# Optimization experiments

Hardware: AMD Instinct MI355X
Metric: run time of the kernel (lower is better)

## Reference

```python
import jax, jax.numpy as jnp
import numpy as np

B, T = 64, 200
NUM_C2 = 2000
NUM_D = 1000
V = 128

# NOTE: Dropout layers are identity in eval mode; this reference implements eval-mode forward.

def setup_inputs() -> dict:
    key = jax.random.key(0)
    ks = jax.random.split(key, 19)
    s = 0.05
    def nrm(k, shape):
        return jax.random.normal(k, shape, jnp.float32) * s
    return {
        "c_seq": jax.random.randint(ks[0], (B, T), 0, NUM_C2),
        "d_seq": jax.random.randint(ks[1], (B, T), 0, NUM_D),
        "r_seq": (jax.random.uniform(ks[2], (B, T)) < 0.5).astype(jnp.float32),
        "D_emb": nrm(ks[3], (NUM_D, 1)),
        "v_d": nrm(ks[4], (V,)),
        "v_r": nrm(ks[5], (V,)),
        "v_c": nrm(ks[6], (V,)),
        "W_ih": nrm(ks[7], (3 * V, 2 * V)),
        "W_hh": nrm(ks[8], (3 * V, V)),
        "b_ih": nrm(ks[9], (3 * V,)),
        "b_hh": nrm(ks[10], (3 * V,)),
        "W1a": nrm(ks[11], (V, V)),
        "b1a": nrm(ks[12], (V,)),
        "W1b": nrm(ks[13], (1, V)),
        "b1b": nrm(ks[14], (1,)),
        "W2a": nrm(ks[15], (V, 3 * V)),
        "b2a": nrm(ks[16], (V,)),
        "W2b": nrm(ks[17], (1, V)),
        "b2b": nrm(ks[18], (1,)),
    }


def reference(c_seq, d_seq, r_seq, D_emb, v_d, v_r, v_c,
              W_ih, W_hh, b_ih, b_hh, W1a, b1a, W1b, b1b,
              W2a, b2a, W2b, b2b):
    gamma_seq = D_emb[d_seq]                 # [B,T,1]
    v_d_seq = gamma_seq * v_d                # [B,T,V]
    v_r_seq = r_seq[..., None] * v_r         # [B,T,V]
    x = jnp.concatenate([v_d_seq, v_r_seq], axis=-1)  # [B,T,2V]

    # --- GRU (PyTorch gate ordering r,z,n), h0 = 0 ---
    def gru_step(h, x_t):
        gi = x_t @ W_ih.T + b_ih
        gh = h @ W_hh.T + b_hh
        i_r, i_z, i_n = jnp.split(gi, 3, axis=-1)
        h_r, h_z, h_n = jnp.split(gh, 3, axis=-1)
        r = jax.nn.sigmoid(i_r + h_r)
        z = jax.nn.sigmoid(i_z + h_z)
        n = jnp.tanh(i_n + r * h_n)
        h_new = (1.0 - z) * n + z * h
        return h_new, h_new

    h0 = jnp.zeros((c_seq.shape[0], v_d.shape[0]), x.dtype)
    _, h_seq = jax.lax.scan(gru_step, h0, jnp.swapaxes(x, 0, 1))
    h_seq = jnp.swapaxes(h_seq, 0, 1)        # [B,T,V]

    # linear_1 (dropout = identity in eval)
    alpha_seq = (jax.nn.relu(h_seq @ W1a.T + b1a) @ W1b.T + b1b)[..., 0]  # [B,T]

    # --- sequential memory update over time ---
    def mem_step(C, inputs):
        c_t, vd_t, vr_t = inputs             # [B], [B,V], [B,V]
        beta = jnp.take_along_axis(C, c_t[:, None], axis=1)   # [B,1]
        vc = beta * v_c                       # [B,V]
        hh = jax.nn.relu(jnp.concatenate([vc, vd_t, vr_t], axis=-1) @ W2a.T + b2a)
        new_c = hh @ W2b.T + b2b              # [B,1]
        oh = jax.nn.one_hot(c_t, C.shape[1], dtype=C.dtype)   # [B,K]
        C_new = C * (1.0 - oh) + new_c * oh
        return C_new, C_new

    C0 = jnp.zeros((c_seq.shape[0], NUM_C2), x.dtype)
    _, C_seq = jax.lax.scan(
        mem_step, C0,
        (jnp.swapaxes(c_seq, 0, 1), jnp.swapaxes(v_d_seq, 0, 1), jnp.swapaxes(v_r_seq, 0, 1)))
    C_seq = jnp.swapaxes(C_seq, 0, 1)[..., None]   # [B,T,K,1]
    return alpha_seq, h_seq, C_seq
```

## Files before the change

kernel.cpp:

```cpp
#include <hip/hip_runtime.h>
#include <hip/hip_bf16.h>
#include <cstdint>

#define BB 64
#define TT 200
#define KN 2000
#define VV 128
#define NGRU 16

typedef __attribute__((ext_vector_type(8))) short bf16x8;
typedef __attribute__((ext_vector_type(4))) float f32x4;
typedef _Float16 half8 __attribute__((ext_vector_type(8)));


__device__ __forceinline__ float sigm(float x) {
    return __builtin_amdgcn_rcpf(1.f + __expf(-x));
}
__device__ __forceinline__ float tanh_f(float x) {
    float e = __expf(2.f * x);
    return 1.f - 2.f * __builtin_amdgcn_rcpf(e + 1.f);
}

__device__ __forceinline__ void soft_barrier() {
    asm volatile("s_waitcnt lgkmcnt(0)" ::: "memory");
    __builtin_amdgcn_s_barrier();
    __builtin_amdgcn_sched_barrier(0);
}

__global__ void pre_kernel(const float* __restrict__ v_d, const float* __restrict__ v_r,
                           const float* __restrict__ v_c, const float* __restrict__ W_ih,
                           const float* __restrict__ W2a, float* __restrict__ ws)
{
    int g = blockIdx.x * 256 + threadIdx.x;
    float* pd = ws;
    float* pr = ws + 384;
    float* uc = ws + 768;
    float* ud = ws + 896;
    float* ur = ws + 1024;
    if (g < 384) {
        float a = 0.f, b = 0.f;
        for (int k = 0; k < VV; ++k) {
            a = fmaf(W_ih[g * 256 + k], v_d[k], a);
            b = fmaf(W_ih[g * 256 + VV + k], v_r[k], b);
        }
        pd[g] = a; pr[g] = b;
    }
    if (g < VV) {
        float a = 0.f, b = 0.f, c = 0.f;
        for (int k = 0; k < VV; ++k) {
            a = fmaf(W2a[g * 384 + k], v_c[k], a);
            b = fmaf(W2a[g * 384 + VV + k], v_d[k], b);
            c = fmaf(W2a[g * 384 + 2 * VV + k], v_r[k], c);
        }
        uc[g] = a; ud[g] = b; ur[g] = c;
    }
}

__device__ __forceinline__ half8 load_cvt8h(const float* p) {
    float4 a = *(const float4*)p;
    float4 c = *(const float4*)(p + 4);
    half8 r;
    r[0] = (_Float16)a.x; r[1] = (_Float16)a.y; r[2] = (_Float16)a.z; r[3] = (_Float16)a.w;
    r[4] = (_Float16)c.x; r[5] = (_Float16)c.y; r[6] = (_Float16)c.z; r[7] = (_Float16)c.w;
    return r;
}

__global__ __launch_bounds__(512, 1) void fused_kernel(
    const int* __restrict__ c_seq, const int* __restrict__ d_seq,
    const float* __restrict__ r_seq, const float* __restrict__ D_emb,
    const float* __restrict__ Whh, const float* __restrict__ bih,
    const float* __restrict__ bhh, const float* __restrict__ W2b,
    const float* __restrict__ b2a, const float* __restrict__ b2b,
    const float* __restrict__ ws, float* __restrict__ C_out,
    float* __restrict__ h_out)
{
    __shared__ __align__(16) _Float16 H_half[16 * 136];
    __shared__ __align__(8) float gam4[TT * 4], r4[TT * 4];
    __shared__ __align__(16) float C[KN];
    __shared__ float gam_row[TT], r_row[TT], n_row[TT];
    __shared__ int c_row[TT + 1];

    int tid = threadIdx.x;

    if (blockIdx.x < NGRU) {
        int b0 = blockIdx.x * 4;
        const float* pd = ws;
        const float* pr = ws + 384;

        for (int i = tid; i < TT * 4; i += 512) {
            int t = i >> 2, rr = i & 3;
            gam4[i] = D_emb[d_seq[(b0 + rr) * TT + t]];
            r4[i] = r_seq[(b0 + rr) * TT + t];
        }
        for (int i = tid; i < 16 * 136; i += 512) H_half[i] = (_Float16)0.f;

        int wid = tid >> 6, l = tid & 63;
        int cl = l & 15, gq = l >> 4;
        int nn = wid * 16 + cl;

        const float* wr = Whh + (size_t)nn * VV + gq * 8;
        const float* wz = Whh + (size_t)(nn + 128) * VV + gq * 8;
        const float* wn = Whh + (size_t)(nn + 256) * VV + gq * 8;
        half8 br0 = load_cvt8h(wr),      br1 = load_cvt8h(wr + 32),
              br2 = load_cvt8h(wr + 64), br3 = load_cvt8h(wr + 96);
        half8 bz0 = load_cvt8h(wz),      bz1 = load_cvt8h(wz + 32),
              bz2 = load_cvt8h(wz + 64), bz3 = load_cvt8h(wz + 96);
        half8 bn0 = load_cvt8h(wn),      bn1 = load_cvt8h(wn + 32),
              bn2 = load_cvt8h(wn + 64), bn3 = load_cvt8h(wn + 96);

        float gr_pd = pd[nn],        gr_pr = pr[nn],        gr_b = bih[nn] + bhh[nn];
        float gz_pd = pd[nn + 128],  gz_pr = pr[nn + 128],  gz_b = bih[nn + 128] + bhh[nn + 128];
        float gn_pd = pd[nn + 256],  gn_pr = pr[nn + 256],  gn_b = bih[nn + 256];
        float gn_bh = bhh[nn + 256];

        float h0 = 0.f;
        __syncthreads();

        for (int t = 0; t < TT; ++t) {
            asm volatile("" : "+v"(br0), "+v"(br1), "+v"(br2), "+v"(br3),
                              "+v"(bz0), "+v"(bz1), "+v"(bz2), "+v"(bz3),
                              "+v"(bn0), "+v"(bn1), "+v"(bn2), "+v"(bn3));
            const int ab = cl * 136 + gq * 8;
            half8 a0 = *(const half8*)&H_half[ab];
            half8 a1 = *(const half8*)&H_half[ab + 32];
            half8 a2 = *(const half8*)&H_half[ab + 64];
            half8 a3 = *(const half8*)&H_half[ab + 96];
            float g1 = gam4[t * 4 + gq];
            float q1 = r4[t * 4 + gq];

            f32x4 z4 = {0.f, 0.f, 0.f, 0.f};
            f32x4 accr = z4, accrh = z4, accz = z4, acczh = z4, accn = z4, accnh = z4;
            accr[0] = fmaf(g1, gr_pd, fmaf(q1, gr_pr, gr_b));
            accz[0] = fmaf(g1, gz_pd, fmaf(q1, gz_pr, gz_b));
            accn[0] = gn_bh;
            float gin0 = fmaf(g1, gn_pd, fmaf(q1, gn_pr, gn_b));

            accr  = __builtin_amdgcn_mfma_f32_16x16x32_f16(a0, br0, accr, 0, 0, 0);
            accrh = __builtin_amdgcn_mfma_f32_16x16x32_f16(a2, br2, accrh, 0, 0, 0);
            accz  = __builtin_amdgcn_mfma_f32_16x16x32_f16(a0, bz0, accz, 0, 0, 0);
            acczh = __builtin_amdgcn_mfma_f32_16x16x32_f16(a2, bz2, acczh, 0, 0, 0);
            accn  = __builtin_amdgcn_mfma_f32_16x16x32_f16(a0, bn0, accn, 0, 0, 0);
            accnh = __builtin_amdgcn_mfma_f32_16x16x32_f16(a2, bn2, accnh, 0, 0, 0);
            accr  = __builtin_amdgcn_mfma_f32_16x16x32_f16(a1, br1, accr, 0, 0, 0);
            accrh = __builtin_amdgcn_mfma_f32_16x16x32_f16(a3, br3, accrh, 0, 0, 0);
            accz  = __builtin_amdgcn_mfma_f32_16x16x32_f16(a1, bz1, accz, 0, 0, 0);
            acczh = __builtin_amdgcn_mfma_f32_16x16x32_f16(a3, bz3, acczh, 0, 0, 0);
            accn  = __builtin_amdgcn_mfma_f32_16x16x32_f16(a1, bn1, accn, 0, 0, 0);
            accnh = __builtin_amdgcn_mfma_f32_16x16x32_f16(a3, bn3, accnh, 0, 0, 0);

            {
                float rg0 = sigm(accr[0] + accrh[0]);
                float zg0 = sigm(accz[0] + acczh[0]);
                float ng0 = tanh_f(fmaf(rg0, accn[0] + accnh[0], gin0));
                h0 = fmaf(1.f - zg0, ng0, zg0 * h0);
                H_half[(gq * 4) * 136 + nn] = (_Float16)h0;
                h_out[((size_t)(b0 + gq) * TT + t) * VV + nn] = h0;
            }
            soft_barrier();
        }
    } else {
        int b = blockIdx.x - NGRU;
        const float* uc = ws + 768;
        const float* ud = ws + 896;
        const float* ur = ws + 1024;
        for (int i = tid; i < KN; i += 512) C[i] = 0.f;
        if (tid < TT) {
            gam_row[tid] = D_emb[d_seq[b * TT + tid]];
            r_row[tid] = r_seq[b * TT + tid];
            c_row[tid] = c_seq[b * TT + tid];
        }
        if (tid == 0) c_row[TT] = 0;
        __syncthreads();

        if (tid < 64) {
            int l = tid;
            float uc0 = uc[l], uc1 = uc[l + 64];
            float ud0 = ud[l], ud1 = ud[l + 64];
            float ur0 = ur[l], ur1 = ur[l + 64];
            float ba0 = b2a[l], ba1 = b2a[l + 64];
            float wb0 = W2b[l], wb1 = W2b[l + 64];
            float bb = b2b[0];
            float beta = 0.f;
            int ct = c_row[0];
            for (int t = 0; t < TT; ++t) {
                int ct1 = c_row[t + 1];
                float cpref = C[ct1];
                float g = gam_row[t], rr = r_row[t];
                float hh0 = fmaxf(fmaf(beta, uc0, fmaf(g, ud0, fmaf(rr, ur0, ba0))), 0.f);
                float hh1 = fmaxf(fmaf(beta, uc1, fmaf(g, ud1, fmaf(rr, ur1, ba1))), 0.f);
                float p = fmaf(hh0, wb0, hh1 * wb1);
                #pragma unroll
                for (int m = 32; m > 0; m >>= 1) p += __shfl_xor(p, m);
                float nc = p + bb;
                if (l == 0) { C[ct] = nc; n_row[t] = nc; }
                beta = (ct1 == ct) ? nc : cpref;
                ct = ct1;
            }
        }
        __syncthreads();

        int k0 = tid * 4;
        if (k0 < KN) {
            float4 cur = {0.f, 0.f, 0.f, 0.f};
            float* cop = C_out + (size_t)b * TT * KN + k0;
            for (int t = 0; t < TT; ++t) {
                int c = c_row[t];
                unsigned d = (unsigned)(c - k0);
                if (d < 4u) {
                    float v = n_row[t];
                    cur.x = (d == 0u) ? v : cur.x;
                    cur.y = (d == 1u) ? v : cur.y;
                    cur.z = (d == 2u) ? v : cur.z;
                    cur.w = (d == 3u) ? v : cur.w;
                }
                *(float4*)(cop + (size_t)t * KN) = cur;
            }
        }
    }
}

__device__ __forceinline__ short f2bf(float f) {
    uint32_t u = __float_as_uint(f);
    u = (u + 0x7FFFu + ((u >> 16) & 1u)) >> 16;
    return (short)u;
}
__device__ __forceinline__ bf16x8 load_cvt8(const float* p) {
    float4 a = *(const float4*)p;
    float4 c = *(const float4*)(p + 4);
    bf16x8 r;
    r[0] = f2bf(a.x); r[1] = f2bf(a.y); r[2] = f2bf(a.z); r[3] = f2bf(a.w);
    r[4] = f2bf(c.x); r[5] = f2bf(c.y); r[6] = f2bf(c.z); r[7] = f2bf(c.w);
    return r;
}

__global__ __launch_bounds__(512) void alpha_kernel(
    const float* __restrict__ h_seq, const float* __restrict__ W1a,
    const float* __restrict__ b1a, const float* __restrict__ W1b,
    const float* __restrict__ b1b, float* __restrict__ alpha)
{
    __shared__ __align__(16) short W1s[128 * 136];
    __shared__ float b1s[128], w1bs[128];
    int tid = threadIdx.x;
    for (int i = tid * 8; i < 128 * 128; i += 512 * 8) {
        int row = i >> 7, col = i & 127;
        *(bf16x8*)&W1s[row * 136 + col] = load_cvt8(W1a + i);
    }
    if (tid < 128) { b1s[tid] = b1a[tid]; w1bs[tid] = W1b[tid]; }
    __syncthreads();

    int wave = tid >> 6, lane = tid & 63;
    int tile = blockIdx.x * 8 + wave;
    int rowbase = tile * 16;
    int rl = lane & 15, g = lane >> 4;
    const float* hp = h_seq + (size_t)(rowbase + rl) * VV + g * 8;
    bf16x8 a0 = load_cvt8(hp);
    bf16x8 a1 = load_cvt8(hp + 32);
    bf16x8 a2 = load_cvt8(hp + 64);
    bf16x8 a3 = load_cvt8(hp + 96);
    float p0 = 0.f, p1 = 0.f, p2 = 0.f, p3 = 0.f;
    float bb = b1b[0];
    #pragma unroll
    for (int jt = 0; jt < 8; ++jt) {
        int j = jt * 16 + rl;
        const short* wp = &W1s[j * 136 + g * 8];
        f32x4 acc = {0.f, 0.f, 0.f, 0.f};
        acc = __builtin_amdgcn_mfma_f32_16x16x32_bf16(a0, *(const bf16x8*)wp, acc, 0, 0, 0);
        acc = __builtin_amdgcn_mfma_f32_16x16x32_bf16(a1, *(const bf16x8*)(wp + 32), acc, 0, 0, 0);
        acc = __builtin_amdgcn_mfma_f32_16x16x32_bf16(a2, *(const bf16x8*)(wp + 64), acc, 0, 0, 0);
        acc = __builtin_amdgcn_mfma_f32_16x16x32_bf16(a3, *(const bf16x8*)(wp + 96), acc, 0, 0, 0);
        float bj = b1s[j], wj = w1bs[j];
        p0 += fmaxf(acc[0] + bj, 0.f) * wj;
        p1 += fmaxf(acc[1] + bj, 0.f) * wj;
        p2 += fmaxf(acc[2] + bj, 0.f) * wj;
        p3 += fmaxf(acc[3] + bj, 0.f) * wj;
    }
    #pragma unroll
    for (int m = 1; m < 16; m <<= 1) {
        p0 += __shfl_xor(p0, m);
        p1 += __shfl_xor(p1, m);
        p2 += __shfl_xor(p2, m);
        p3 += __shfl_xor(p3, m);
    }
    if (rl == 0) {
        alpha[rowbase + g * 4 + 0] = p0 + bb;
        alpha[rowbase + g * 4 + 1] = p1 + bb;
        alpha[rowbase + g * 4 + 2] = p2 + bb;
        alpha[rowbase + g * 4 + 3] = p3 + bb;
    }
}

extern "C" void kernel_launch(void* const* d_in, const int* in_sizes, int n_in,
                              void* d_out, int out_size, void* d_ws, size_t ws_size,
                              hipStream_t stream)
{
    const int*   c_seq = (const int*)d_in[0];
    const int*   d_seq = (const int*)d_in[1];
    const float* r_seq = (const float*)d_in[2];
    const float* D_emb = (const float*)d_in[3];
    const float* v_d   = (const float*)d_in[4];
    const float* v_r   = (const float*)d_in[5];
    const float* v_c   = (const float*)d_in[6];
    const float* W_ih  = (const float*)d_in[7];
    const float* W_hh  = (const float*)d_in[8];
    const float* b_ih  = (const float*)d_in[9];
    const float* b_hh  = (const float*)d_in[10];
    const float* W1a   = (const float*)d_in[11];
    const float* b1a   = (const float*)d_in[12];
    const float* W1b   = (const float*)d_in[13];
    const float* b1b   = (const float*)d_in[14];
    const float* W2a   = (const float*)d_in[15];
    const float* b2a   = (const float*)d_in[16];
    const float* W2b   = (const float*)d_in[17];
    const float* b2b   = (const float*)d_in[18];

    float* out   = (float*)d_out;
    float* alpha = out;
    float* h_seq = out + 12800;
    float* C_out = out + 12800 + 1638400;
    float* ws    = (float*)d_ws;

    hipLaunchKernelGGL(pre_kernel, dim3(2), dim3(256), 0, stream,
                       v_d, v_r, v_c, W_ih, W2a, ws);
    hipLaunchKernelGGL(fused_kernel, dim3(NGRU + BB), dim3(512), 0, stream,
                       c_seq, d_seq, r_seq, D_emb, W_hh, b_ih, b_hh,
                       W2b, b2a, b2b, ws, C_out, h_seq);
    hipLaunchKernelGGL(alpha_kernel, dim3(100), dim3(512), 0, stream,
                       h_seq, W1a, b1a, W1b, b1b, alpha);
}
```

Measured before the change: 117.8 us.

## Halve GRU block size with two hidden-column tiles per wave

New measurement: 136.5 us. 15.9% more time.

```diff
diff --git a/kernel.cpp b/kernel.cpp
--- a/kernel.cpp
+++ b/kernel.cpp
@@ -65,7 +65,7 @@
     return r;
 }
 
-__global__ __launch_bounds__(512, 1) void fused_kernel(
+__global__ __launch_bounds__(256, 1) void fused_kernel(
     const int* __restrict__ c_seq, const int* __restrict__ d_seq,
     const float* __restrict__ r_seq, const float* __restrict__ D_emb,
     const float* __restrict__ Whh, const float* __restrict__ bih,
@@ -87,39 +87,58 @@
         const float* pd = ws;
         const float* pr = ws + 384;
 
-        for (int i = tid; i < TT * 4; i += 512) {
+        for (int i = tid; i < TT * 4; i += 256) {
             int t = i >> 2, rr = i & 3;
             gam4[i] = D_emb[d_seq[(b0 + rr) * TT + t]];
             r4[i] = r_seq[(b0 + rr) * TT + t];
         }
-        for (int i = tid; i < 16 * 136; i += 512) H_half[i] = (_Float16)0.f;
+        for (int i = tid; i < 16 * 136; i += 256) H_half[i] = (_Float16)0.f;
 
         int wid = tid >> 6, l = tid & 63;
         int cl = l & 15, gq = l >> 4;
-        int nn = wid * 16 + cl;
-
-        const float* wr = Whh + (size_t)nn * VV + gq * 8;
-        const float* wz = Whh + (size_t)(nn + 128) * VV + gq * 8;
-        const float* wn = Whh + (size_t)(nn + 256) * VV + gq * 8;
-        half8 br0 = load_cvt8h(wr),      br1 = load_cvt8h(wr + 32),
-              br2 = load_cvt8h(wr + 64), br3 = load_cvt8h(wr + 96);
-        half8 bz0 = load_cvt8h(wz),      bz1 = load_cvt8h(wz + 32),
-              bz2 = load_cvt8h(wz + 64), bz3 = load_cvt8h(wz + 96);
-        half8 bn0 = load_cvt8h(wn),      bn1 = load_cvt8h(wn + 32),
-              bn2 = load_cvt8h(wn + 64), bn3 = load_cvt8h(wn + 96);
-
-        float gr_pd = pd[nn],        gr_pr = pr[nn],        gr_b = bih[nn] + bhh[nn];
-        float gz_pd = pd[nn + 128],  gz_pr = pr[nn + 128],  gz_b = bih[nn + 128] + bhh[nn + 128];
-        float gn_pd = pd[nn + 256],  gn_pr = pr[nn + 256],  gn_b = bih[nn + 256];
-        float gn_bh = bhh[nn + 256];
-
-        float h0 = 0.f;
+        int c1 = wid * 32 + cl;
+        int c2 = c1 + 16;
+
+        const float* wr1 = Whh + (size_t)c1 * VV + gq * 8;
+        const float* wz1 = Whh + (size_t)(c1 + 128) * VV + gq * 8;
+        const float* wn1 = Whh + (size_t)(c1 + 256) * VV + gq * 8;
+        const float* wr2 = Whh + (size_t)c2 * VV + gq * 8;
+        const float* wz2 = Whh + (size_t)(c2 + 128) * VV + gq * 8;
+        const float* wn2 = Whh + (size_t)(c2 + 256) * VV + gq * 8;
+        half8 br10 = load_cvt8h(wr1),      br11 = load_cvt8h(wr1 + 32),
+              br12 = load_cvt8h(wr1 + 64), br13 = load_cvt8h(wr1 + 96);
+        half8 bz10 = load_cvt8h(wz1),      bz11 = load_cvt8h(wz1 + 32),
+              bz12 = load_cvt8h(wz1 + 64), bz13 = load_cvt8h(wz1 + 96);
+        half8 bn10 = load_cvt8h(wn1),      bn11 = load_cvt8h(wn1 + 32),
+              bn12 = load_cvt8h(wn1 + 64), bn13 = load_cvt8h(wn1 + 96);
+        half8 br20 = load_cvt8h(wr2),      br21 = load_cvt8h(wr2 + 32),
+              br22 = load_cvt8h(wr2 + 64), br23 = load_cvt8h(wr2 + 96);
+        half8 bz20 = load_cvt8h(wz2),      bz21 = load_cvt8h(wz2 + 32),
+              bz22 = load_cvt8h(wz2 + 64), bz23 = load_cvt8h(wz2 + 96);
+        half8 bn20 = load_cvt8h(wn2),      bn21 = load_cvt8h(wn2 + 32),
+              bn22 = load_cvt8h(wn2 + 64), bn23 = load_cvt8h(wn2 + 96);
+
+        float gr_pd1 = pd[c1],       gr_pr1 = pr[c1],       gr_b1 = bih[c1] + bhh[c1];
+        float gz_pd1 = pd[c1 + 128], gz_pr1 = pr[c1 + 128], gz_b1 = bih[c1 + 128] + bhh[c1 + 128];
+        float gn_pd1 = pd[c1 + 256], gn_pr1 = pr[c1 + 256], gn_b1 = bih[c1 + 256];
+        float gn_bh1 = bhh[c1 + 256];
+        float gr_pd2 = pd[c2],       gr_pr2 = pr[c2],       gr_b2 = bih[c2] + bhh[c2];
+        float gz_pd2 = pd[c2 + 128], gz_pr2 = pr[c2 + 128], gz_b2 = bih[c2 + 128] + bhh[c2 + 128];
+        float gn_pd2 = pd[c2 + 256], gn_pr2 = pr[c2 + 256], gn_b2 = bih[c2 + 256];
+        float gn_bh2 = bhh[c2 + 256];
+
+        float h1 = 0.f, h2 = 0.f;
         __syncthreads();
 
+        float* hp = h_out + ((size_t)(b0 + gq) * TT) * VV;
+
         for (int t = 0; t < TT; ++t) {
-            asm volatile("" : "+v"(br0), "+v"(br1), "+v"(br2), "+v"(br3),
-                              "+v"(bz0), "+v"(bz1), "+v"(bz2), "+v"(bz3),
-                              "+v"(bn0), "+v"(bn1), "+v"(bn2), "+v"(bn3));
+            asm volatile("" : "+v"(br10), "+v"(br11), "+v"(br12), "+v"(br13),
+                              "+v"(bz10), "+v"(bz11), "+v"(bz12), "+v"(bz13),
+                              "+v"(bn10), "+v"(bn11), "+v"(bn12), "+v"(bn13));
+            asm volatile("" : "+v"(br20), "+v"(br21), "+v"(br22), "+v"(br23),
+                              "+v"(bz20), "+v"(bz21), "+v"(bz22), "+v"(bz23),
+                              "+v"(bn20), "+v"(bn21), "+v"(bn22), "+v"(bn23));
             const int ab = cl * 136 + gq * 8;
             half8 a0 = *(const half8*)&H_half[ab];
             half8 a1 = *(const half8*)&H_half[ab + 32];
@@ -129,32 +148,55 @@
             float q1 = r4[t * 4 + gq];
 
             f32x4 z4 = {0.f, 0.f, 0.f, 0.f};
-            f32x4 accr = z4, accrh = z4, accz = z4, acczh = z4, accn = z4, accnh = z4;
-            accr[0] = fmaf(g1, gr_pd, fmaf(q1, gr_pr, gr_b));
-            accz[0] = fmaf(g1, gz_pd, fmaf(q1, gz_pr, gz_b));
-            accn[0] = gn_bh;
-            float gin0 = fmaf(g1, gn_pd, fmaf(q1, gn_pr, gn_b));
-
-            accr  = __builtin_amdgcn_mfma_f32_16x16x32_f16(a0, br0, accr, 0, 0, 0);
-            accrh = __builtin_amdgcn_mfma_f32_16x16x32_f16(a2, br2, accrh, 0, 0, 0);
-            accz  = __builtin_amdgcn_mfma_f32_16x16x32_f16(a0, bz0, accz, 0, 0, 0);
-            acczh = __builtin_amdgcn_mfma_f32_16x16x32_f16(a2, bz2, acczh, 0, 0, 0);
-            accn  = __builtin_amdgcn_mfma_f32_16x16x32_f16(a0, bn0, accn, 0, 0, 0);
-            accnh = __builtin_amdgcn_mfma_f32_16x16x32_f16(a2, bn2, accnh, 0, 0, 0);
-            accr  = __builtin_amdgcn_mfma_f32_16x16x32_f16(a1, br1, accr, 0, 0, 0);
-            accrh = __builtin_amdgcn_mfma_f32_16x16x32_f16(a3, br3, accrh, 0, 0, 0);
-            accz  = __builtin_amdgcn_mfma_f32_16x16x32_f16(a1, bz1, accz, 0, 0, 0);
-            acczh = __builtin_amdgcn_mfma_f32_16x16x32_f16(a3, bz3, acczh, 0, 0, 0);
-            accn  = __builtin_amdgcn_mfma_f32_16x16x32_f16(a1, bn1, accn, 0, 0, 0);
-            accnh = __builtin_amdgcn_mfma_f32_16x16x32_f16(a3, bn3, accnh, 0, 0, 0);
+            f32x4 accr1 = z4, accz1 = z4, accn1 = z4;
+            f32x4 accr2 = z4, accz2 = z4, accn2 = z4;
+            accr1[0] = fmaf(g1, gr_pd1, fmaf(q1, gr_pr1, gr_b1));
+            accz1[0] = fmaf(g1, gz_pd1, fmaf(q1, gz_pr1, gz_b1));
+            accn1[0] = gn_bh1;
+            float gin1 = fmaf(g1, gn_pd1, fmaf(q1, gn_pr1, gn_b1));
+            accr2[0] = fmaf(g1, gr_pd2, fmaf(q1, gr_pr2, gr_b2));
+            accz2[0] = fmaf(g1, gz_pd2, fmaf(q1, gz_pr2, gz_b2));
+            accn2[0] = gn_bh2;
+            float gin2 = fmaf(g1, gn_pd2, fmaf(q1, gn_pr2, gn_b2));
+
+            accr1 = __builtin_amdgcn_mfma_f32_16x16x32_f16(a0, br10, accr1, 0, 0, 0);
+            accr1 = __builtin_amdgcn_mfma_f32_16x16x32_f16(a1, br11, accr1, 0, 0, 0);
+            accr1 = __builtin_amdgcn_mfma_f32_16x16x32_f16(a2, br12, accr1, 0, 0, 0);
+            accr1 = __builtin_amdgcn_mfma_f32_16x16x32_f16(a3, br13, accr1, 0, 0, 0);
+            accz1 = __builtin_amdgcn_mfma_f32_16x16x32_f16(a0, bz10, accz1, 0, 0, 0);
+            accz1 = __builtin_amdgcn_mfma_f32_16x16x32_f16(a1, bz11, accz1, 0, 0, 0);
+            accz1 = __builtin_amdgcn_mfma_f32_16x16x32_f16(a2, bz12, accz1, 0, 0, 0);
+            accz1 = __builtin_amdgcn_mfma_f32_16x16x32_f16(a3, bz13, accz1, 0, 0, 0);
+            accn1 = __builtin_amdgcn_mfma_f32_16x16x32_f16(a0, bn10, accn1, 0, 0, 0);
+            accn1 = __builtin_amdgcn_mfma_f32_16x16x32_f16(a1, bn11, accn1, 0, 0, 0);
+            accn1 = __builtin_amdgcn_mfma_f32_16x16x32_f16(a2, bn12, accn1, 0, 0, 0);
+            accn1 = __builtin_amdgcn_mfma_f32_16x16x32_f16(a3, bn13, accn1, 0, 0, 0);
+            accr2 = __builtin_amdgcn_mfma_f32_16x16x32_f16(a0, br20, accr2, 0, 0, 0);
+            accr2 = __builtin_amdgcn_mfma_f32_16x16x32_f16(a1, br21, accr2, 0, 0, 0);
+            accr2 = __builtin_amdgcn_mfma_f32_16x16x32_f16(a2, br22, accr2, 0, 0, 0);
+            accr2 = __builtin_amdgcn_mfma_f32_16x16x32_f16(a3, br23, accr2, 0, 0, 0);
+            accz2 = __builtin_amdgcn_mfma_f32_16x16x32_f16(a0, bz20, accz2, 0, 0, 0);
+            accz2 = __builtin_amdgcn_mfma_f32_16x16x32_f16(a1, bz21, accz2, 0, 0, 0);
+            accz2 = __builtin_amdgcn_mfma_f32_16x16x32_f16(a2, bz22, accz2, 0, 0, 0);
+            accz2 = __builtin_amdgcn_mfma_f32_16x16x32_f16(a3, bz23, accz2, 0, 0, 0);
+            accn2 = __builtin_amdgcn_mfma_f32_16x16x32_f16(a0, bn20, accn2, 0, 0, 0);
+            accn2 = __builtin_amdgcn_mfma_f32_16x16x32_f16(a1, bn21, accn2, 0, 0, 0);
+            accn2 = __builtin_amdgcn_mfma_f32_16x16x32_f16(a2, bn22, accn2, 0, 0, 0);
+            accn2 = __builtin_amdgcn_mfma_f32_16x16x32_f16(a3, bn23, accn2, 0, 0, 0);
 
             {
-                float rg0 = sigm(accr[0] + accrh[0]);
-                float zg0 = sigm(accz[0] + acczh[0]);
-                float ng0 = tanh_f(fmaf(rg0, accn[0] + accnh[0], gin0));
-                h0 = fmaf(1.f - zg0, ng0, zg0 * h0);
-                H_half[(gq * 4) * 136 + nn] = (_Float16)h0;
-                h_out[((size_t)(b0 + gq) * TT + t) * VV + nn] = h0;
+                float rg1 = sigm(accr1[0]);
+                float zg1 = sigm(accz1[0]);
+                float ng1 = tanh_f(fmaf(rg1, accn1[0], gin1));
+                h1 = fmaf(1.f - zg1, ng1, zg1 * h1);
+                float rg2 = sigm(accr2[0]);
+                float zg2 = sigm(accz2[0]);
+                float ng2 = tanh_f(fmaf(rg2, accn2[0], gin2));
+                h2 = fmaf(1.f - zg2, ng2, zg2 * h2);
+                H_half[(gq * 4) * 136 + c1] = (_Float16)h1;
+                H_half[(gq * 4) * 136 + c2] = (_Float16)h2;
+                hp[t * VV + c1] = h1;
+                hp[t * VV + c2] = h2;
             }
             soft_barrier();
         }
@@ -163,7 +205,7 @@
         const float* uc = ws + 768;
         const float* ud = ws + 896;
         const float* ur = ws + 1024;
-        for (int i = tid; i < KN; i += 512) C[i] = 0.f;
+        for (int i = tid; i < KN; i += 256) C[i] = 0.f;
         if (tid < TT) {
             gam_row[tid] = D_emb[d_seq[b * TT + tid]];
             r_row[tid] = r_seq[b * TT + tid];
@@ -199,21 +241,27 @@
         }
         __syncthreads();
 
-        int k0 = tid * 4;
+        int k0 = tid * 8;
         if (k0 < KN) {
-            float4 cur = {0.f, 0.f, 0.f, 0.f};
+            float4 cur0 = {0.f, 0.f, 0.f, 0.f};
+            float4 cur1 = {0.f, 0.f, 0.f, 0.f};
             float* cop = C_out + (size_t)b * TT * KN + k0;
             for (int t = 0; t < TT; ++t) {
                 int c = c_row[t];
                 unsigned d = (unsigned)(c - k0);
-                if (d < 4u) {
+                if (d < 8u) {
                     float v = n_row[t];
-                    cur.x = (d == 0u) ? v : cur.x;
-                    cur.y = (d == 1u) ? v : cur.y;
-                    cur.z = (d == 2u) ? v : cur.z;
-                    cur.w = (d == 3u) ? v : cur.w;
+                    cur0.x = (d == 0u) ? v : cur0.x;
+                    cur0.y = (d == 1u) ? v : cur0.y;
+                    cur0.z = (d == 2u) ? v : cur0.z;
+                    cur0.w = (d == 3u) ? v : cur0.w;
+                    cur1.x = (d == 4u) ? v : cur1.x;
+                    cur1.y = (d == 5u) ? v : cur1.y;
+                    cur1.z = (d == 6u) ? v : cur1.z;
+                    cur1.w = (d == 7u) ? v : cur1.w;
                 }
-                *(float4*)(cop + (size_t)t * KN) = cur;
+                *(float4*)(cop + (size_t)t * KN) = cur0;
+                *(float4*)(cop + (size_t)t * KN + 4) = cur1;
             }
         }
     }
@@ -321,7 +369,7 @@
 
     hipLaunchKernelGGL(pre_kernel, dim3(2), dim3(256), 0, stream,
                        v_d, v_r, v_c, W_ih, W2a, ws);
-    hipLaunchKernelGGL(fused_kernel, dim3(NGRU + BB), dim3(512), 0, stream,
+    hipLaunchKernelGGL(fused_kernel, dim3(NGRU + BB), dim3(256), 0, stream,
                        c_seq, d_seq, r_seq, D_emb, W_hh, b_ih, b_hh,
                        W2b, b2a, b2b, ws, C_out, h_seq);
     hipLaunchKernelGGL(alpha_kernel, dim3(100), dim3(512), 0, stream,
```
